# Kernel optimization log

Hardware: AMD Instinct MI355X
Metric: run time of the kernel (lower is better)

## Reference

```python
import jax, jax.numpy as jnp
import numpy as np

BATCH = 256
SIZE = 512      # must be a power of two for the bitonic network
K = 16          # top-k
STEEPNESS = 10.0  # cauchy distribution scale (module default)


def _bitonic_layers(n):
    """Static index pairs of the bitonic sorting network (ascending).
    Returns (lefts, rights), each int32 [n_layers, n//2]. After a compare-swap,
    the soft-min goes to `left` and the soft-max goes to `right`."""
    lefts, rights = [], []
    k = 2
    while k <= n:
        j = k // 2
        while j >= 1:
            l_idx, r_idx = [], []
            for i in range(n):
                l = i ^ j
                if l > i:
                    if (i & k) == 0:   # ascending block: min at i
                        l_idx.append(i); r_idx.append(l)
                    else:              # descending block: min at l
                        l_idx.append(l); r_idx.append(i)
            lefts.append(l_idx); rights.append(r_idx)
            j //= 2
        k *= 2
    return np.asarray(lefts, np.int32), np.asarray(rights, np.int32)


def setup_inputs() -> dict:
    key = jax.random.key(0)
    vectors = jax.random.normal(key, (BATCH, SIZE), dtype=jnp.float32)
    return {"vectors": vectors}


def reference(vectors):
    b, n = vectors.shape
    lefts_np, rights_np = _bitonic_layers(n)
    lefts = jnp.asarray(lefts_np)
    rights = jnp.asarray(rights_np)
    # soft permutation matrix: X[b, i, j] = P(input j ends at sorted pos i)
    X0 = jnp.broadcast_to(jnp.eye(n, dtype=vectors.dtype)[None], (b, n, n))

    def step(carry, lr):
        x, X = carry
        l, r = lr                      # [n//2] index pairs for this layer
        a = x[:, l]                    # [b, n//2]
        c = x[:, r]
        # cauchy CDF of steepness*(c - a): prob that no swap is needed
        alpha = jnp.arctan((c - a) * STEEPNESS) / jnp.pi + 0.5
        x = x.at[:, l].set(alpha * a + (1.0 - alpha) * c)
        x = x.at[:, r].set(alpha * c + (1.0 - alpha) * a)
        Xl = X[:, l, :]                # [b, n//2, n]
        Xr = X[:, r, :]
        al = alpha[..., None]
        X = X.at[:, l, :].set(al * Xl + (1.0 - al) * Xr)
        X = X.at[:, r, :].set(al * Xr + (1.0 - al) * Xl)
        return (x, X), None

    (_, X), _ = jax.lax.scan(step, (vectors, X0), (lefts, rights))
    # ascending sort -> last K rows correspond to the K largest elements;
    # flip so row 0 = largest. Output: [batch, K, n] soft top-k distribution.
    return jnp.flip(X[:, n - K:, :], axis=1)
```

## Files before the change

kernel.cpp:

```cpp
#include <hip/hip_runtime.h>
#include <math.h>

#define N 512
#define BATCH 256
#define KTOP 16
#define NLAYERS 45
#define NPAIRS 256

__device__ __forceinline__ float fast_alpha(float t) {
    const float at  = __builtin_fabsf(t);
    const bool inv  = at > 1.0f;
    const float z   = inv ? __builtin_amdgcn_rcpf(at) : at;
    const float s   = z * z;
    float p = -0.0117212f;
    p = __builtin_fmaf(p, s,  0.05265332f);
    p = __builtin_fmaf(p, s, -0.11643287f);
    p = __builtin_fmaf(p, s,  0.19354346f);
    p = __builtin_fmaf(p, s, -0.33262347f);
    p = __builtin_fmaf(p, s,  0.99997726f);
    float r = z * p;
    r = inv ? (1.5707963267948966f - r) : r;
    r = (t < 0.0f) ? -r : r;
    return __builtin_fmaf(r, 0.3183098861837907f, 0.5f);
}

__global__ __launch_bounds__(512, 2)
void difftopk_kernel(const float* __restrict__ x_in, float* __restrict__ out) {
    __shared__ float xs[2][N];
    __shared__ __align__(16) float As[NLAYERS][NPAIRS];

    const int b    = blockIdx.x;
    const int e    = threadIdx.x;
    const int lane = e & 63;

    float o = x_in[(size_t)b * N + e];

    int t = 0, par = 0;
    #pragma unroll 1
    for (int s = 1; s <= 9; ++s) {
        const int k  = 1 << s;
        const bool kb = (e & k) == 0;
        #pragma unroll 1
        for (int lg = s - 1; lg >= 0; --lg, ++t) {
            const int j = 1 << lg;
            float p;
            if (lg >= 6) {
                xs[par][e] = o;
                __syncthreads();
                p = xs[par][e ^ j];
                par ^= 1;
            } else {
                p = __shfl_xor(o, j, 64);
            }
            const bool jb = (e & j) == 0;
            const float d = (kb == jb) ? (p - o) : (o - p);
            const float alpha = fast_alpha(d * 10.0f);
            o = __builtin_fmaf(alpha, o - p, p);
            if (jb) {
                const int ord = ((e >> (lg + 1)) << lg) | (e & (j - 1));
                As[t][ord] = alpha;
            }
        }
    }
    __syncthreads();

    const int wave  = e >> 6;
    const int lane8 = lane << 3;
    const int r0 = N - 1 - wave;
    const int r1 = N - 1 - (wave + 8);

    float v0[8], v1[8];
    #pragma unroll
    for (int m = 0; m < 8; ++m) {
        v0[m] = (lane8 + m == r0) ? 1.0f : 0.0f;
        v1[m] = (lane8 + m == r1) ? 1.0f : 0.0f;
    }

    #pragma unroll 1
    for (int s = 9; s >= 1; --s) {
        const int base = (s * (s - 1)) >> 1;
        #pragma unroll 1
        for (int lg = 0; lg < s; ++lg) {
            const int tt = base + (s - 1 - lg);
            if (lg >= 3) {
                const int j    = 1 << lg;
                const int ordb = ((lane8 >> (lg + 1)) << lg) | (lane8 & (j - 1));
                const float4 a0 = *(const float4*)&As[tt][ordb];
                const float4 a1 = *(const float4*)&As[tt][ordb + 4];
                const float al[8] = {a0.x, a0.y, a0.z, a0.w, a1.x, a1.y, a1.z, a1.w};
                const int lm = j >> 3;
                #pragma unroll
                for (int m = 0; m < 8; ++m) {
                    const float p0 = __shfl_xor(v0[m], lm, 64);
                    const float p1 = __shfl_xor(v1[m], lm, 64);
                    v0[m] = __builtin_fmaf(al[m], v0[m] - p0, p0);
                    v1[m] = __builtin_fmaf(al[m], v1[m] - p1, p1);
                }
            } else {
                const float4 a = *(const float4*)&As[tt][lane << 2];
                const float aa[4] = {a.x, a.y, a.z, a.w};
                float n0[8], n1[8];
                if (lg == 2) {
                    #pragma unroll
                    for (int m = 0; m < 8; ++m) {
                        const float al = aa[m & 3];
                        n0[m] = __builtin_fmaf(al, v0[m] - v0[m ^ 4], v0[m ^ 4]);
                        n1[m] = __builtin_fmaf(al, v1[m] - v1[m ^ 4], v1[m ^ 4]);
                    }
                } else if (lg == 1) {
                    #pragma unroll
                    for (int m = 0; m < 8; ++m) {
                        const float al = aa[((m >> 2) << 1) | (m & 1)];
                        n0[m] = __builtin_fmaf(al, v0[m] - v0[m ^ 2], v0[m ^ 2]);
                        n1[m] = __builtin_fmaf(al, v1[m] - v1[m ^ 2], v1[m ^ 2]);
                    }
                } else {
                    #pragma unroll
                    for (int m = 0; m < 8; ++m) {
                        const float al = aa[m >> 1];
                        n0[m] = __builtin_fmaf(al, v0[m] - v0[m ^ 1], v0[m ^ 1]);
                        n1[m] = __builtin_fmaf(al, v1[m] - v1[m ^ 1], v1[m ^ 1]);
                    }
                }
                #pragma unroll
                for (int m = 0; m < 8; ++m) { v0[m] = n0[m]; v1[m] = n1[m]; }
            }
        }
    }

    float4* dst0 = (float4*)(out + ((size_t)b * KTOP + wave) * N + lane8);
    dst0[0] = make_float4(v0[0], v0[1], v0[2], v0[3]);
    dst0[1] = make_float4(v0[4], v0[5], v0[6], v0[7]);
    float4* dst1 = (float4*)(out + ((size_t)b * KTOP + wave + 8) * N + lane8);
    dst1[0] = make_float4(v1[0], v1[1], v1[2], v1[3]);
    dst1[1] = make_float4(v1[4], v1[5], v1[6], v1[7]);
}

extern "C" void kernel_launch(void* const* d_in, const int* in_sizes, int n_in,
                              void* d_out, int out_size, void* d_ws, size_t ws_size,
                              hipStream_t stream) {
    const float* x = (const float*)d_in[0];
    float* out = (float*)d_out;
    difftopk_kernel<<<dim3(BATCH), dim3(512), 0, stream>>>(x, out);
}
```

Before: 78.74 us.

## Backward pass: 4 waves each hold 4 rows x 32 columns per lane

The backward propagation of the top-K rows is remapped so only 4 waves do the work. Each lane holds 32 contiguous columns of one output row, and 16 lanes cover a row, so more butterfly layers (j<32) are done in registers without cross-lane shuffles. Launch bounds are relaxed to 1 block per SM to allow the larger register footprint. The trade-off is half the waves being idle in the backward phase and possibly lower occupancy, in exchange for fewer shuffles and fewer LDS alpha reads per element.

```diff
diff --git a/kernel.cpp b/kernel.cpp
--- a/kernel.cpp
+++ b/kernel.cpp
@@ -24,14 +24,13 @@
     return __builtin_fmaf(r, 0.3183098861837907f, 0.5f);
 }
 
-__global__ __launch_bounds__(512, 2)
+__global__ __launch_bounds__(512, 1)
 void difftopk_kernel(const float* __restrict__ x_in, float* __restrict__ out) {
     __shared__ float xs[2][N];
     __shared__ __align__(16) float As[NLAYERS][NPAIRS];
 
     const int b    = blockIdx.x;
     const int e    = threadIdx.x;
-    const int lane = e & 63;
 
     float o = x_in[(size_t)b * N + e];
 
@@ -64,17 +63,19 @@
     }
     __syncthreads();
 
-    const int wave  = e >> 6;
-    const int lane8 = lane << 3;
-    const int r0 = N - 1 - wave;
-    const int r1 = N - 1 - (wave + 8);
+    const int w = e >> 6;
+    if (w >= 4) return;
 
-    float v0[8], v1[8];
+    const int lane = e & 63;
+    const int g    = lane >> 4;
+    const int h    = lane & 15;
+    const int kk   = (w << 2) | g;
+    const int r    = N - 1 - kk;
+    const int p0   = h << 5;
+
+    float v[32];
     #pragma unroll
-    for (int m = 0; m < 8; ++m) {
-        v0[m] = (lane8 + m == r0) ? 1.0f : 0.0f;
-        v1[m] = (lane8 + m == r1) ? 1.0f : 0.0f;
-    }
+    for (int m = 0; m < 32; ++m) v[m] = (p0 + m == r) ? 1.0f : 0.0f;
 
     #pragma unroll 1
     for (int s = 9; s >= 1; --s) {
@@ -82,58 +83,83 @@
         #pragma unroll 1
         for (int lg = 0; lg < s; ++lg) {
             const int tt = base + (s - 1 - lg);
-            if (lg >= 3) {
+            if (lg >= 5) {
                 const int j    = 1 << lg;
-                const int ordb = ((lane8 >> (lg + 1)) << lg) | (lane8 & (j - 1));
-                const float4 a0 = *(const float4*)&As[tt][ordb];
-                const float4 a1 = *(const float4*)&As[tt][ordb + 4];
-                const float al[8] = {a0.x, a0.y, a0.z, a0.w, a1.x, a1.y, a1.z, a1.w};
-                const int lm = j >> 3;
+                const int ordb = ((p0 >> (lg + 1)) << lg) | (p0 & (j - 1));
+                float al[32];
                 #pragma unroll
-                for (int m = 0; m < 8; ++m) {
-                    const float p0 = __shfl_xor(v0[m], lm, 64);
-                    const float p1 = __shfl_xor(v1[m], lm, 64);
-                    v0[m] = __builtin_fmaf(al[m], v0[m] - p0, p0);
-                    v1[m] = __builtin_fmaf(al[m], v1[m] - p1, p1);
+                for (int q = 0; q < 8; ++q) {
+                    const float4 a = *(const float4*)&As[tt][ordb + (q << 2)];
+                    al[4*q] = a.x; al[4*q+1] = a.y; al[4*q+2] = a.z; al[4*q+3] = a.w;
+                }
+                const int mask = j >> 5;
+                #pragma unroll
+                for (int m = 0; m < 32; ++m) {
+                    const float pt = __shfl_xor(v[m], mask, 64);
+                    v[m] = __builtin_fmaf(al[m], v[m] - pt, pt);
                 }
             } else {
-                const float4 a = *(const float4*)&As[tt][lane << 2];
-                const float aa[4] = {a.x, a.y, a.z, a.w};
-                float n0[8], n1[8];
-                if (lg == 2) {
+                float aa[16];
+                #pragma unroll
+                for (int q = 0; q < 4; ++q) {
+                    const float4 a = *(const float4*)&As[tt][(h << 4) + (q << 2)];
+                    aa[4*q] = a.x; aa[4*q+1] = a.y; aa[4*q+2] = a.z; aa[4*q+3] = a.w;
+                }
+                switch (lg) {
+                case 4:
                     #pragma unroll
-                    for (int m = 0; m < 8; ++m) {
-                        const float al = aa[m & 3];
-                        n0[m] = __builtin_fmaf(al, v0[m] - v0[m ^ 4], v0[m ^ 4]);
-                        n1[m] = __builtin_fmaf(al, v1[m] - v1[m ^ 4], v1[m ^ 4]);
+                    for (int i = 0; i < 16; ++i) {
+                        const int lo = i, hi = i | 16;
+                        const float x0 = v[lo], x1 = v[hi], a = aa[i];
+                        v[lo] = __builtin_fmaf(a, x0 - x1, x1);
+                        v[hi] = __builtin_fmaf(a, x1 - x0, x0);
                     }
-                } else if (lg == 1) {
+                    break;
+                case 3:
                     #pragma unroll
-                    for (int m = 0; m < 8; ++m) {
-                        const float al = aa[((m >> 2) << 1) | (m & 1)];
-                        n0[m] = __builtin_fmaf(al, v0[m] - v0[m ^ 2], v0[m ^ 2]);
-                        n1[m] = __builtin_fmaf(al, v1[m] - v1[m ^ 2], v1[m ^ 2]);
+                    for (int i = 0; i < 16; ++i) {
+                        const int lo = ((i >> 3) << 4) | (i & 7), hi = lo | 8;
+                        const float x0 = v[lo], x1 = v[hi], a = aa[i];
+                        v[lo] = __builtin_fmaf(a, x0 - x1, x1);
+                        v[hi] = __builtin_fmaf(a, x1 - x0, x0);
                     }
-                } else {
+                    break;
+                case 2:
                     #pragma unroll
-                    for (int m = 0; m < 8; ++m) {
-                        const float al = aa[m >> 1];
-                        n0[m] = __builtin_fmaf(al, v0[m] - v0[m ^ 1], v0[m ^ 1]);
-                        n1[m] = __builtin_fmaf(al, v1[m] - v1[m ^ 1], v1[m ^ 1]);
+                    for (int i = 0; i < 16; ++i) {
+                        const int lo = ((i >> 2) << 3) | (i & 3), hi = lo | 4;
+                        const float x0 = v[lo], x1 = v[hi], a = aa[i];
+                        v[lo] = __builtin_fmaf(a, x0 - x1, x1);
+                        v[hi] = __builtin_fmaf(a, x1 - x0, x0);
                     }
+                    break;
+                case 1:
+                    #pragma unroll
+                    for (int i = 0; i < 16; ++i) {
+                        const int lo = ((i >> 1) << 2) | (i & 1), hi = lo | 2;
+                        const float x0 = v[lo], x1 = v[hi], a = aa[i];
+                        v[lo] = __builtin_fmaf(a, x0 - x1, x1);
+                        v[hi] = __builtin_fmaf(a, x1 - x0, x0);
+                    }
+                    break;
+                default:
+                    #pragma unroll
+                    for (int i = 0; i < 16; ++i) {
+                        const int lo = i << 1, hi = lo | 1;
+                        const float x0 = v[lo], x1 = v[hi], a = aa[i];
+                        v[lo] = __builtin_fmaf(a, x0 - x1, x1);
+                        v[hi] = __builtin_fmaf(a, x1 - x0, x0);
+                    }
+                    break;
                 }
-                #pragma unroll
-                for (int m = 0; m < 8; ++m) { v0[m] = n0[m]; v1[m] = n1[m]; }
             }
         }
     }
 
-    float4* dst0 = (float4*)(out + ((size_t)b * KTOP + wave) * N + lane8);
-    dst0[0] = make_float4(v0[0], v0[1], v0[2], v0[3]);
-    dst0[1] = make_float4(v0[4], v0[5], v0[6], v0[7]);
-    float4* dst1 = (float4*)(out + ((size_t)b * KTOP + wave + 8) * N + lane8);
-    dst1[0] = make_float4(v1[0], v1[1], v1[2], v1[3]);
-    dst1[1] = make_float4(v1[4], v1[5], v1[6], v1[7]);
+    float* dst = out + ((size_t)b * KTOP + kk) * N + p0;
+    #pragma unroll
+    for (int q = 0; q < 8; ++q)
+        *(float4*)(dst + (q << 2)) = make_float4(v[4*q], v[4*q+1], v[4*q+2], v[4*q+3]);
 }
 
 extern "C" void kernel_launch(void* const* d_in, const int* in_sizes, int n_in,
```

Result: slower. 84.47 us (+7.3%).
